# Kernel optimization log

Measured on AMD Instinct MI355X. Metric: run time of the kernel, lower is better.

## Reference

```python
import jax, jax.numpy as jnp
import numpy as np

RES = 64

TRI_TABLE = jnp.array([
    [-1,-1,-1,-1,-1,-1],[1,0,2,-1,-1,-1],[4,0,3,-1,-1,-1],[1,4,2,1,3,4],
    [3,1,5,-1,-1,-1],[2,3,0,2,5,3],[1,4,0,1,5,4],[4,2,5,-1,-1,-1],
    [4,5,2,-1,-1,-1],[4,1,0,4,5,1],[3,2,0,3,5,2],[1,3,5,-1,-1,-1],
    [4,1,2,4,3,1],[3,0,4,-1,-1,-1],[2,0,1,-1,-1,-1],[-1,-1,-1,-1,-1,-1]], dtype=jnp.int32)
NUM_TRI = jnp.array([0,1,1,2,1,2,2,1,1,2,2,1,2,1,1,0], dtype=jnp.int32)
BASE_EDGES = jnp.array([0,1,0,2,0,3,1,2,1,3,2,3], dtype=jnp.int32)


def _make_tet_grid(res):
    # Kuhn 6-tet decomposition of each cube of a (res+1)^3 grid.
    n = res + 1
    ii, jj, kk = np.meshgrid(np.arange(n), np.arange(n), np.arange(n), indexing='ij')
    verts = (np.stack([ii, jj, kk], -1).reshape(-1, 3).astype(np.float32)) / res
    def vid(i, j, k):
        return (i * n + j) * n + k
    i, j, k = np.meshgrid(np.arange(res), np.arange(res), np.arange(res), indexing='ij')
    i, j, k = i.ravel(), j.ravel(), k.ravel()
    c = [vid(i + (b & 1), j + ((b >> 1) & 1), k + ((b >> 2) & 1)) for b in range(8)]
    kuhn = [(0,1,3,7),(0,3,2,7),(0,2,6,7),(0,6,4,7),(0,4,5,7),(0,5,1,7)]
    tets = np.stack([np.stack([c[a], c[b], c[d], c[e]], -1) for (a, b, d, e) in kuhn], 1)
    return verts, tets.reshape(-1, 4).astype(np.int64)


def setup_inputs() -> dict:
    key = jax.random.key(0)
    verts, tets = _make_tet_grid(RES)
    level = jax.random.normal(key, (verts.shape[0], 1), dtype=jnp.float32)
    return {"level": level, "pos": jnp.asarray(verts), "tet": jnp.asarray(tets), "threshold": 0}


def reference(level, pos, tet, threshold):
    sdf = level - threshold                    # [N,1]
    occ = sdf[:, 0] > 0                        # [N]
    occ_fx4 = occ[tet]                         # [F,4]
    occ_sum = occ_fx4.sum(-1)
    valid = (occ_sum > 0) & (occ_sum < 4)
    vt = tet[valid]                            # [Fv,4]
    occ_valid = occ_fx4[valid]                 # [Fv,4]

    edges = jnp.sort(vt[:, BASE_EDGES].reshape(-1, 2), axis=1)   # [Fv*6,2]
    unique_edges, idx_map = jnp.unique(edges, axis=0, return_inverse=True)
    idx_map = idx_map.reshape(-1)
    mask_edges = occ[unique_edges].sum(-1) == 1                  # crossing edges
    mapping = jnp.where(mask_edges, jnp.cumsum(mask_edges) - 1, -1)
    idx_map = mapping[idx_map].reshape(-1, 6)                    # [Fv,6]
    interp_v = unique_edges[mask_edges]                          # [M,2]

    p = pos[interp_v]                                            # [M,2,3]
    s = sdf[interp_v][..., 0] * jnp.array([1.0, -1.0], dtype=sdf.dtype)  # [M,2]
    w = s[:, ::-1] / s.sum(1, keepdims=True)                     # flip / denom
    verts_out = (p * w[..., None]).sum(1)                        # [M,3]

    v_id = 2 ** jnp.arange(4, dtype=jnp.int32)
    tetindex = (occ_valid.astype(jnp.int32) * v_id).sum(-1)      # [Fv]
    num_tri = NUM_TRI[tetindex]
    m1, m2 = num_tri == 1, num_tri == 2
    f1 = jnp.take_along_axis(idx_map[m1], TRI_TABLE[tetindex[m1]][:, :3], axis=1).reshape(-1, 3)
    f2 = jnp.take_along_axis(idx_map[m2], TRI_TABLE[tetindex[m2]][:, :6], axis=1).reshape(-1, 3)
    faces = jnp.concatenate([f1, f2], axis=0)
    return verts_out, faces
```

## Files before the change

### kernel.cpp

```cpp
#include <hip/hip_runtime.h>


#define RESX 64
#define NV   65
#define NV2  4225
#define NVERT 274625
#define NCUBE 262144
#define BLOCK 256
#define NBLK 1073
#define CBLK 1024

__constant__ int c_tri[16][6] = {
    {-1,-1,-1,-1,-1,-1},{1,0,2,-1,-1,-1},{4,0,3,-1,-1,-1},{1,4,2,1,3,4},
    {3,1,5,-1,-1,-1},{2,3,0,2,5,3},{1,4,0,1,5,4},{4,2,5,-1,-1,-1},
    {4,5,2,-1,-1,-1},{4,1,0,4,5,1},{3,2,0,3,5,2},{1,3,5,-1,-1,-1},
    {4,1,2,4,3,1},{3,0,4,-1,-1,-1},{2,0,1,-1,-1,-1},{-1,-1,-1,-1,-1,-1}};
__constant__ int c_ntri[16] = {0,1,1,2,1,2,2,1,1,2,2,1,2,1,1,0};
__constant__ int c_kuhn[6][4] = {{0,1,3,7},{0,3,2,7},{0,2,6,7},{0,6,4,7},{0,4,5,7},{0,5,1,7}};
__constant__ int c_off8[8] = {0,4225,65,4290,1,4226,66,4291};
__constant__ int c_loc[6][6] = {
    {0,0,0,1,1,3},{0,0,0,2,3,2},{0,0,0,2,2,6},
    {0,0,0,4,6,4},{0,0,0,4,4,5},{0,0,0,1,5,1}};
__constant__ int c_dir[6][6] = {
    {3,5,6,1,2,0},{5,1,6,3,0,4},{1,2,6,0,4,3},
    {2,0,6,1,3,5},{0,4,6,3,5,1},{4,3,6,0,1,2}};

__device__ __forceinline__ unsigned block_reduce(unsigned v, unsigned* lds) {
    int tid = threadIdx.x, lane = tid & 63, w = tid >> 6;
#pragma unroll
    for (int off = 32; off > 0; off >>= 1)
        v += (unsigned)__shfl_xor((int)v, off, 64);
    if (lane == 0) lds[w] = v;
    __syncthreads();
    if (tid == 0) lds[4] = lds[0] + lds[1] + lds[2] + lds[3];
    __syncthreads();
    return lds[4];
}

__device__ __forceinline__ unsigned block_scan_excl(unsigned val, unsigned* lds,
                                                    unsigned& block_total) {
    int tid = threadIdx.x, lane = tid & 63, w = tid >> 6;
    unsigned x = val;
#pragma unroll
    for (int off = 1; off < 64; off <<= 1) {
        unsigned y = (unsigned)__shfl_up((int)x, off, 64);
        if (lane >= off) x += y;
    }
    if (lane == 63) lds[w] = x;
    __syncthreads();
    if (tid == 0) {
        unsigned s = 0;
#pragma unroll
        for (int i = 0; i < 4; i++) { unsigned t = lds[i]; lds[i + 4] = s; s += t; }
        lds[8] = s;
    }
    __syncthreads();
    block_total = lds[8];
    return x - val + lds[4 + w];
}

__global__ void pass1(const float* __restrict__ level, const float* __restrict__ thrp,
                      unsigned char* __restrict__ flagsArr,
                      unsigned* __restrict__ bsE,
                      unsigned* __restrict__ bs1, unsigned* __restrict__ bs2) {
    __shared__ unsigned ldsA[5], ldsB[5];
    int tid = threadIdx.x;
    int gid = blockIdx.x * BLOCK + tid;
    float thr = thrp[0];
    unsigned cnt = 0;
    if (gid < NVERT) {
        int i = gid / NV2; int r = gid - i * NV2; int j = r / NV; int k = r - j * NV;
        bool okx = i < RESX, oky = j < RESX, okz = k < RESX;
        float v0 = level[gid] - thr;
        bool s0 = v0 > 0.f;
        unsigned fl = s0 ? 0x80u : 0u;
        const int b2d[8] = {0, 3, 1, 5, 0, 4, 2, 6};
#pragma unroll
        for (int b = 1; b < 8; b++) {
            bool ok = (!(b & 1) || okx) && (!(b & 2) || oky) && (!(b & 4) || okz);
            if (ok) {
                float vb = level[gid + c_off8[b]] - thr;
                if ((vb > 0.f) != s0) fl |= (1u << b2d[b]);
            }
        }
        flagsArr[gid] = (unsigned char)fl;
        cnt = __popc(fl & 0x7fu);
    }
    unsigned totE = block_reduce(cnt, ldsA);
    unsigned tv = 0;
    if (gid < NCUBE) {
        int ci = gid >> 12, cj = (gid >> 6) & 63, ck = gid & 63;
        int base = (ci * NV + cj) * NV + ck;
        unsigned occ8 = 0;
#pragma unroll
        for (int b = 0; b < 8; b++)
            occ8 |= ((level[base + c_off8[b]] - thr) > 0.f ? 1u : 0u) << b;
        unsigned c1 = 0, c2 = 0;
#pragma unroll
        for (int t = 0; t < 6; t++) {
            int cfg = ((occ8 >> c_kuhn[t][0]) & 1) | (((occ8 >> c_kuhn[t][1]) & 1) << 1)
                    | (((occ8 >> c_kuhn[t][2]) & 1) << 2) | (((occ8 >> c_kuhn[t][3]) & 1) << 3);
            int nt = c_ntri[cfg];
            c1 += (nt == 1); c2 += (nt == 2);
        }
        tv = c1 | (c2 << 16);
    }
    unsigned totT = block_reduce(tv, ldsB);
    if (tid == 0) {
        bsE[blockIdx.x] = totE;
        bs1[blockIdx.x] = totT & 0xffffu;
        bs2[blockIdx.x] = totT >> 16;
    }
}

__global__ void scan_partials(unsigned* bsE, unsigned* bs1, unsigned* bs2,
                              unsigned* totals) {
    __shared__ unsigned lds[9];
    unsigned* arr = (blockIdx.x == 0) ? bsE : (blockIdx.x == 1 ? bs1 : bs2);
    unsigned running = 0;
    for (int base = 0; base < NBLK; base += BLOCK) {
        int idx = base + threadIdx.x;
        unsigned v = (idx < NBLK) ? arr[idx] : 0u;
        unsigned tot;
        unsigned ex = block_scan_excl(v, lds, tot);
        if (idx < NBLK) arr[idx] = running + ex;
        running += tot;
        __syncthreads();
    }
    if (threadIdx.x == 0) totals[blockIdx.x] = running;
}

__global__ void emit_verts(const float* __restrict__ level,
                           const float* __restrict__ thrp,
                           const unsigned* __restrict__ bsE,
                           unsigned* __restrict__ base_rank,
                           float* __restrict__ out) {
    __shared__ unsigned lds[9];
    int tid = threadIdx.x;
    int gid = blockIdx.x * BLOCK + tid;
    float thr = thrp[0];
    float v0 = 0.f;
    bool s0 = false;
    float vals[8];
    unsigned fl = 0;
    int i = 0, j = 0, k = 0;
    if (gid < NVERT) {
        i = gid / NV2; int r = gid - i * NV2; j = r / NV; k = r - j * NV;
        bool okx = i < RESX, oky = j < RESX, okz = k < RESX;
        v0 = level[gid] - thr; s0 = v0 > 0.f;
        vals[0] = v0;
        const int b2d[8] = {0, 3, 1, 5, 0, 4, 2, 6};
#pragma unroll
        for (int b = 1; b < 8; b++) {
            bool ok = (!(b & 1) || okx) && (!(b & 2) || oky) && (!(b & 4) || okz);
            float vb = ok ? (level[gid + c_off8[b]] - thr) : 0.f;
            vals[b] = vb;
            if (ok && ((vb > 0.f) != s0)) fl |= (1u << b2d[b]);
        }
    }
    unsigned cnt = __popc(fl & 0x7fu);
    unsigned tot;
    unsigned ex = block_scan_excl(cnt, lds, tot);
    unsigned rank = bsE[blockIdx.x] + ex;
    if (gid < NVERT) base_rank[gid] = rank;
    if (fl & 0x7fu) {
        const float inv = 1.f / 64.f;
        const int d2b[7] = {4, 2, 6, 1, 5, 3, 7};
        float fi = (float)i, fj = (float)j, fk = (float)k;
#pragma unroll
        for (int d = 0; d < 7; d++) {
            if (fl & (1u << d)) {
                const int b = d2b[d];
                float s1 = vals[b];
                float denom = v0 - s1;
                float w0 = (-s1) / denom;
                float w1 = v0 / denom;
                float* o = out + 3u * rank;
                o[0] = (fi * w0 + (fi + (float)(b & 1)) * w1) * inv;
                o[1] = (fj * w0 + (fj + (float)((b >> 1) & 1)) * w1) * inv;
                o[2] = (fk * w0 + (fk + (float)((b >> 2) & 1)) * w1) * inv;
                rank++;
            }
        }
    }
}

__global__ void emit_faces(const unsigned char* __restrict__ flagsArr,
                           const unsigned* __restrict__ base_rank,
                           const unsigned* __restrict__ bs1,
                           const unsigned* __restrict__ bs2,
                           const unsigned* __restrict__ totals,
                           float* __restrict__ out) {
    __shared__ unsigned lds[9];
    int tid = threadIdx.x;
    int gid = blockIdx.x * BLOCK + tid;
    int ci = gid >> 12, cj = (gid >> 6) & 63, ck = gid & 63;
    int base = (ci * NV + cj) * NV + ck;
    unsigned long long f8 = 0ull;
#pragma unroll
    for (int b = 0; b < 8; b++)
        f8 |= (unsigned long long)flagsArr[base + c_off8[b]] << (8 * b);
    unsigned occ8 = 0;
#pragma unroll
    for (int b = 0; b < 8; b++) occ8 |= (unsigned)((f8 >> (8 * b + 7)) & 1ull) << b;
    int cfgs[6], nts[6];
    unsigned c1 = 0, c2 = 0;
#pragma unroll
    for (int t = 0; t < 6; t++) {
        int cfg = ((occ8 >> c_kuhn[t][0]) & 1) | (((occ8 >> c_kuhn[t][1]) & 1) << 1)
                | (((occ8 >> c_kuhn[t][2]) & 1) << 2) | (((occ8 >> c_kuhn[t][3]) & 1) << 3);
        cfgs[t] = cfg;
        int nt = c_ntri[cfg];
        nts[t] = nt;
        c1 += (nt == 1); c2 += (nt == 2);
    }
    unsigned tot;
    unsigned ex = block_scan_excl(c1 | (c2 << 16), lds, tot);
    unsigned p1 = bs1[blockIdx.x] + (ex & 0xffffu);
    unsigned p2 = bs2[blockIdx.x] + (ex >> 16);
    unsigned M = totals[0], C1 = totals[1];
    float* of = out + 3ull * M;
#pragma unroll
    for (int t = 0; t < 6; t++) {
        int nt = nts[t];
        if (nt == 0) continue;
        int cfg = cfgs[t];
        unsigned tri0 = (nt == 1) ? p1 : (C1 + 2u * p2);
        int cntm = 3 * nt;
        for (int m = 0; m < cntm; m++) {
            int e = c_tri[cfg][m];
            int lc = c_loc[t][e];
            int dir = c_dir[t][e];
            int lo = base + c_off8[lc];
            unsigned flb = (unsigned)((f8 >> (8 * lc)) & 0xffull);
            unsigned rank = base_rank[lo] + __popc(flb & ((1u << dir) - 1u));
            of[3u * tri0 + (unsigned)m] = (float)rank;
        }
        p1 += (nt == 1);
        p2 += (nt == 2);
    }
}

extern "C" void kernel_launch(void* const* d_in, const int* in_sizes, int n_in,
                              void* d_out, int out_size, void* d_ws, size_t ws_size,
                              hipStream_t stream) {
    const float* level = (const float*)d_in[0];
    const float* thrp = (const float*)d_in[3];
    float* out = (float*)d_out;

    unsigned char* flagsArr = (unsigned char*)d_ws;
    unsigned* u = (unsigned*)((char*)d_ws + ((NVERT + 255) & ~255));
    unsigned* base_rank = u;
    unsigned* bsE = base_rank + NVERT;
    unsigned* bs1 = bsE + NBLK;
    unsigned* bs2 = bs1 + NBLK;
    unsigned* totals = bs2 + NBLK;

    pass1<<<NBLK, BLOCK, 0, stream>>>(level, thrp, flagsArr, bsE, bs1, bs2);
    scan_partials<<<3, BLOCK, 0, stream>>>(bsE, bs1, bs2, totals);
    emit_verts<<<NBLK, BLOCK, 0, stream>>>(level, thrp, bsE, base_rank, out);
    emit_faces<<<CBLK, BLOCK, 0, stream>>>(flagsArr, base_rank, bs1, bs2, totals, out);
}
```

Baseline: 131.1 us.

## Fuse count, scan and vertex emission into one decoupled-lookback kernel

Merges the counting pass, the separate partial-sum scan kernel and the vertex emission kernel into a single kernel. Blocks publish their edge and triangle counts through status-tagged 64-bit descriptors and compute exclusive prefixes with a wave-wide decoupled lookback. This removes two kernel launches and the second read of the level grid. In exchange it needs a memset of the descriptors and relies on blocks being scheduled in forward order so that spin-waiting cannot deadlock.

```diff
diff --git a/kernel.cpp b/kernel.cpp
--- a/kernel.cpp
+++ b/kernel.cpp
@@ -9,6 +9,8 @@
 #define BLOCK 256
 #define NBLK 1073
 #define CBLK 1024
+
+typedef unsigned long long u64;
 
 __constant__ int c_tri[16][6] = {
     {-1,-1,-1,-1,-1,-1},{1,0,2,-1,-1,-1},{4,0,3,-1,-1,-1},{1,4,2,1,3,4},
@@ -25,6 +27,20 @@
     {3,5,6,1,2,0},{5,1,6,3,0,4},{1,2,6,0,4,3},
     {2,0,6,1,3,5},{0,4,6,3,5,1},{4,3,6,0,1,2}};
 
+__device__ __forceinline__ u64 ld_acq(u64* p) {
+    return __hip_atomic_load(p, __ATOMIC_ACQUIRE, __HIP_MEMORY_SCOPE_AGENT);
+}
+__device__ __forceinline__ void st_rel(u64* p, u64 v) {
+    __hip_atomic_store(p, v, __ATOMIC_RELEASE, __HIP_MEMORY_SCOPE_AGENT);
+}
+
+__device__ __forceinline__ unsigned wave_reduce_add(unsigned v) {
+#pragma unroll
+    for (int off = 32; off; off >>= 1)
+        v += (unsigned)__shfl_xor((int)v, off, 64);
+    return v;
+}
+
 __device__ __forceinline__ unsigned block_reduce(unsigned v, unsigned* lds) {
     int tid = threadIdx.x, lane = tid & 63, w = tid >> 6;
 #pragma unroll
@@ -59,34 +75,79 @@
     return x - val + lds[4 + w];
 }
 
-__global__ void pass1(const float* __restrict__ level, const float* __restrict__ thrp,
-                      unsigned char* __restrict__ flagsArr,
-                      unsigned* __restrict__ bsE,
-                      unsigned* __restrict__ bs1, unsigned* __restrict__ bs2) {
-    __shared__ unsigned ldsA[5], ldsB[5];
+__device__ u64 lookback(u64* desc, int bid, u64 own) {
+    int lane = threadIdx.x & 63;
+    if (bid == 0) {
+        if (lane == 0) st_rel(&desc[0], (2ull << 62) | own);
+        return 0;
+    }
+    if (lane == 0) st_rel(&desc[bid], (1ull << 62) | own);
+    u64 excl = 0;
+    int b = bid;
+    for (;;) {
+        int idx = b - 1 - lane;
+        u64 d;
+        if (idx < 0) d = (2ull << 62);
+        else do { d = ld_acq(&desc[idx]); } while ((d >> 62) == 0);
+        unsigned lo = (unsigned)(d & 0x1fffffu);
+        unsigned hi = (unsigned)((d >> 21) & 0x1fffffu);
+        u64 pmask = __ballot((d >> 62) == 2ull);
+        if (pmask) {
+            int p = __ffsll(pmask) - 1;
+            unsigned ulo = (lane <= p) ? lo : 0u;
+            unsigned uhi = (lane <= p) ? hi : 0u;
+            ulo = wave_reduce_add(ulo);
+            uhi = wave_reduce_add(uhi);
+            excl += (u64)ulo | ((u64)uhi << 21);
+            break;
+        }
+        unsigned ulo = wave_reduce_add(lo);
+        unsigned uhi = wave_reduce_add(hi);
+        excl += (u64)ulo | ((u64)uhi << 21);
+        b -= 64;
+    }
+    if (lane == 0) st_rel(&desc[bid], (2ull << 62) | (excl + own));
+    return excl;
+}
+
+__global__ void __launch_bounds__(256)
+kernelA(const float* __restrict__ level, const float* __restrict__ thrp,
+        unsigned char* __restrict__ flagsArr, unsigned* __restrict__ base_rank,
+        unsigned* __restrict__ bs1, unsigned* __restrict__ bs2,
+        unsigned* __restrict__ totals, u64* descE, u64* descC,
+        float* __restrict__ out) {
+    __shared__ unsigned lds[9];
+    __shared__ unsigned ldsc[5];
+    __shared__ unsigned eexcl_sh;
     int tid = threadIdx.x;
     int gid = blockIdx.x * BLOCK + tid;
     float thr = thrp[0];
-    unsigned cnt = 0;
+
+    float vals[8];
+    unsigned fl = 0;
+    float v0 = 0.f;
+    int i = 0, j = 0, k = 0;
     if (gid < NVERT) {
-        int i = gid / NV2; int r = gid - i * NV2; int j = r / NV; int k = r - j * NV;
+        i = gid / NV2; int r = gid - i * NV2; j = r / NV; k = r - j * NV;
         bool okx = i < RESX, oky = j < RESX, okz = k < RESX;
-        float v0 = level[gid] - thr;
+        v0 = level[gid] - thr;
         bool s0 = v0 > 0.f;
-        unsigned fl = s0 ? 0x80u : 0u;
+        vals[0] = v0;
+        fl = s0 ? 0x80u : 0u;
         const int b2d[8] = {0, 3, 1, 5, 0, 4, 2, 6};
 #pragma unroll
         for (int b = 1; b < 8; b++) {
             bool ok = (!(b & 1) || okx) && (!(b & 2) || oky) && (!(b & 4) || okz);
-            if (ok) {
-                float vb = level[gid + c_off8[b]] - thr;
-                if ((vb > 0.f) != s0) fl |= (1u << b2d[b]);
-            }
+            float vb = ok ? (level[gid + c_off8[b]] - thr) : 0.f;
+            vals[b] = vb;
+            if (ok && ((vb > 0.f) != s0)) fl |= (1u << b2d[b]);
         }
         flagsArr[gid] = (unsigned char)fl;
-        cnt = __popc(fl & 0x7fu);
-    }
-    unsigned totE = block_reduce(cnt, ldsA);
+    }
+    unsigned cnt = __popc(fl & 0x7fu);
+    unsigned totE;
+    unsigned ex = block_scan_excl(cnt, lds, totE);
+
     unsigned tv = 0;
     if (gid < NCUBE) {
         int ci = gid >> 12, cj = (gid >> 6) & 63, ck = gid & 63;
@@ -105,63 +166,28 @@
         }
         tv = c1 | (c2 << 16);
     }
-    unsigned totT = block_reduce(tv, ldsB);
-    if (tid == 0) {
-        bsE[blockIdx.x] = totE;
-        bs1[blockIdx.x] = totT & 0xffffu;
-        bs2[blockIdx.x] = totT >> 16;
-    }
-}
-
-__global__ void scan_partials(unsigned* bsE, unsigned* bs1, unsigned* bs2,
-                              unsigned* totals) {
-    __shared__ unsigned lds[9];
-    unsigned* arr = (blockIdx.x == 0) ? bsE : (blockIdx.x == 1 ? bs1 : bs2);
-    unsigned running = 0;
-    for (int base = 0; base < NBLK; base += BLOCK) {
-        int idx = base + threadIdx.x;
-        unsigned v = (idx < NBLK) ? arr[idx] : 0u;
-        unsigned tot;
-        unsigned ex = block_scan_excl(v, lds, tot);
-        if (idx < NBLK) arr[idx] = running + ex;
-        running += tot;
-        __syncthreads();
-    }
-    if (threadIdx.x == 0) totals[blockIdx.x] = running;
-}
-
-__global__ void emit_verts(const float* __restrict__ level,
-                           const float* __restrict__ thrp,
-                           const unsigned* __restrict__ bsE,
-                           unsigned* __restrict__ base_rank,
-                           float* __restrict__ out) {
-    __shared__ unsigned lds[9];
-    int tid = threadIdx.x;
-    int gid = blockIdx.x * BLOCK + tid;
-    float thr = thrp[0];
-    float v0 = 0.f;
-    bool s0 = false;
-    float vals[8];
-    unsigned fl = 0;
-    int i = 0, j = 0, k = 0;
-    if (gid < NVERT) {
-        i = gid / NV2; int r = gid - i * NV2; j = r / NV; k = r - j * NV;
-        bool okx = i < RESX, oky = j < RESX, okz = k < RESX;
-        v0 = level[gid] - thr; s0 = v0 > 0.f;
-        vals[0] = v0;
-        const int b2d[8] = {0, 3, 1, 5, 0, 4, 2, 6};
-#pragma unroll
-        for (int b = 1; b < 8; b++) {
-            bool ok = (!(b & 1) || okx) && (!(b & 2) || oky) && (!(b & 4) || okz);
-            float vb = ok ? (level[gid + c_off8[b]] - thr) : 0.f;
-            vals[b] = vb;
-            if (ok && ((vb > 0.f) != s0)) fl |= (1u << b2d[b]);
-        }
-    }
-    unsigned cnt = __popc(fl & 0x7fu);
-    unsigned tot;
-    unsigned ex = block_scan_excl(cnt, lds, tot);
-    unsigned rank = bsE[blockIdx.x] + ex;
+    unsigned totC = block_reduce(tv, ldsc);
+
+    int w = tid >> 6;
+    if (w == 0) {
+        u64 e = lookback(descE, blockIdx.x, (u64)totE);
+        if ((tid & 63) == 0) {
+            eexcl_sh = (unsigned)e;
+            if (blockIdx.x == NBLK - 1) totals[0] = (unsigned)e + totE;
+        }
+    } else if (w == 1 && blockIdx.x < CBLK) {
+        u64 pay = (u64)(totC & 0xffffu) | ((u64)(totC >> 16) << 21);
+        u64 c = lookback(descC, blockIdx.x, pay);
+        if ((tid & 63) == 0) {
+            bs1[blockIdx.x] = (unsigned)(c & 0x1fffffu);
+            bs2[blockIdx.x] = (unsigned)((c >> 21) & 0x1fffffu);
+            if (blockIdx.x == CBLK - 1)
+                totals[1] = (unsigned)((c + pay) & 0x1fffffu);
+        }
+    }
+    __syncthreads();
+
+    unsigned rank = eexcl_sh + ex;
     if (gid < NVERT) base_rank[gid] = rank;
     if (fl & 0x7fu) {
         const float inv = 1.f / 64.f;
@@ -185,12 +211,11 @@
     }
 }
 
-__global__ void emit_faces(const unsigned char* __restrict__ flagsArr,
-                           const unsigned* __restrict__ base_rank,
-                           const unsigned* __restrict__ bs1,
-                           const unsigned* __restrict__ bs2,
-                           const unsigned* __restrict__ totals,
-                           float* __restrict__ out) {
+__global__ void __launch_bounds__(256)
+emit_faces(const unsigned char* __restrict__ flagsArr,
+           const unsigned* __restrict__ base_rank,
+           const unsigned* __restrict__ bs1, const unsigned* __restrict__ bs2,
+           const unsigned* __restrict__ totals, float* __restrict__ out) {
     __shared__ unsigned lds[9];
     int tid = threadIdx.x;
     int gid = blockIdx.x * BLOCK + tid;
@@ -248,16 +273,22 @@
     const float* thrp = (const float*)d_in[3];
     float* out = (float*)d_out;
 
-    unsigned char* flagsArr = (unsigned char*)d_ws;
-    unsigned* u = (unsigned*)((char*)d_ws + ((NVERT + 255) & ~255));
-    unsigned* base_rank = u;
-    unsigned* bsE = base_rank + NVERT;
-    unsigned* bs1 = bsE + NBLK;
-    unsigned* bs2 = bs1 + NBLK;
-    unsigned* totals = bs2 + NBLK;
-
-    pass1<<<NBLK, BLOCK, 0, stream>>>(level, thrp, flagsArr, bsE, bs1, bs2);
-    scan_partials<<<3, BLOCK, 0, stream>>>(bsE, bs1, bs2, totals);
-    emit_verts<<<NBLK, BLOCK, 0, stream>>>(level, thrp, bsE, base_rank, out);
-    emit_faces<<<CBLK, BLOCK, 0, stream>>>(flagsArr, base_rank, bs1, bs2, totals, out);
-}
+    char* p = (char*)d_ws;
+    unsigned char* flagsArr = (unsigned char*)p;
+    p += (NVERT + 255) & ~255;
+    unsigned* base_rank = (unsigned*)p; p += sizeof(unsigned) * NVERT;
+    unsigned* bs1 = (unsigned*)p;       p += sizeof(unsigned) * CBLK;
+    unsigned* bs2 = (unsigned*)p;       p += sizeof(unsigned) * CBLK;
+    p = (char*)(((uintptr_t)p + 7) & ~(uintptr_t)7);
+    char* zero_base = p;
+    u64* descE = (u64*)p;               p += sizeof(u64) * NBLK;
+    u64* descC = (u64*)p;               p += sizeof(u64) * CBLK;
+    unsigned* totals = (unsigned*)p;    p += sizeof(unsigned) * 8;
+    size_t zbytes = (size_t)(p - zero_base);
+
+    hipMemsetAsync(zero_base, 0, zbytes, stream);
+    kernelA<<<NBLK, BLOCK, 0, stream>>>(level, thrp, flagsArr, base_rank,
+                                        bs1, bs2, totals, descE, descC, out);
+    emit_faces<<<CBLK, BLOCK, 0, stream>>>(flagsArr, base_rank, bs1, bs2,
+                                           totals, out);
+}
```

After: 288.9 us. +120.3%, slower.

## Fuse partial scan and emit kernels into two-pass scheme with per-block redundant reductions

Applied to the files above, without the earlier changes.

Collapses four launches into two. The first pass stores each vertex's in-block exclusive edge offset as a 16-bit value next to the block totals. The second pass has every block redundantly reduce all block partials to get its own prefixes and the global counts, then emits vertices and faces in the same kernel. Face ranks come from a small shared window of block prefixes plus the local offsets, so the 32-bit base_rank array and the separate scan kernel are no longer needed. The cost is redundant partial-sum reads in every block and the assumption that the face neighbourhood spans at most WINW vertex blocks.

```diff
diff --git a/kernel.cpp b/kernel.cpp
--- a/kernel.cpp
+++ b/kernel.cpp
@@ -9,6 +9,7 @@
 #define BLOCK 256
 #define NBLK 1073
 #define CBLK 1024
+#define WINW 20
 
 __constant__ int c_tri[16][6] = {
     {-1,-1,-1,-1,-1,-1},{1,0,2,-1,-1,-1},{4,0,3,-1,-1,-1},{1,4,2,1,3,4},
@@ -59,21 +60,24 @@
     return x - val + lds[4 + w];
 }
 
-__global__ void pass1(const float* __restrict__ level, const float* __restrict__ thrp,
-                      unsigned char* __restrict__ flagsArr,
-                      unsigned* __restrict__ bsE,
-                      unsigned* __restrict__ bs1, unsigned* __restrict__ bs2) {
-    __shared__ unsigned ldsA[5], ldsB[5];
+__global__ void __launch_bounds__(256)
+pass1(const float* __restrict__ level, const float* __restrict__ thrp,
+      unsigned char* __restrict__ flagsArr, unsigned short* __restrict__ locEx,
+      unsigned* __restrict__ bsE, unsigned* __restrict__ bsT) {
+    __shared__ unsigned lds[9];
+    __shared__ unsigned ldsc[5];
     int tid = threadIdx.x;
-    int gid = blockIdx.x * BLOCK + tid;
+    int bid = blockIdx.x;
+    int gid = bid * BLOCK + tid;
     float thr = thrp[0];
-    unsigned cnt = 0;
+
+    unsigned fl = 0;
     if (gid < NVERT) {
         int i = gid / NV2; int r = gid - i * NV2; int j = r / NV; int k = r - j * NV;
         bool okx = i < RESX, oky = j < RESX, okz = k < RESX;
         float v0 = level[gid] - thr;
         bool s0 = v0 > 0.f;
-        unsigned fl = s0 ? 0x80u : 0u;
+        fl = s0 ? 0x80u : 0u;
         const int b2d[8] = {0, 3, 1, 5, 0, 4, 2, 6};
 #pragma unroll
         for (int b = 1; b < 8; b++) {
@@ -84,9 +88,13 @@
             }
         }
         flagsArr[gid] = (unsigned char)fl;
-        cnt = __popc(fl & 0x7fu);
-    }
-    unsigned totE = block_reduce(cnt, ldsA);
+    }
+    unsigned cnt = __popc(fl & 0x7fu);
+    unsigned totE;
+    unsigned ex = block_scan_excl(cnt, lds, totE);
+    if (gid < NVERT) locEx[gid] = (unsigned short)ex;
+    if (tid == 0) bsE[bid] = totE;
+
     unsigned tv = 0;
     if (gid < NCUBE) {
         int ci = gid >> 12, cj = (gid >> 6) & 63, ck = gid & 63;
@@ -105,95 +113,80 @@
         }
         tv = c1 | (c2 << 16);
     }
-    unsigned totT = block_reduce(tv, ldsB);
-    if (tid == 0) {
-        bsE[blockIdx.x] = totE;
-        bs1[blockIdx.x] = totT & 0xffffu;
-        bs2[blockIdx.x] = totT >> 16;
-    }
-}
-
-__global__ void scan_partials(unsigned* bsE, unsigned* bs1, unsigned* bs2,
-                              unsigned* totals) {
+    unsigned totC = block_reduce(tv, ldsc);
+    if (tid == 0) bsT[bid] = totC;
+}
+
+__global__ void __launch_bounds__(256)
+pass2(const float* __restrict__ level, const float* __restrict__ thrp,
+      const unsigned char* __restrict__ flagsArr,
+      const unsigned short* __restrict__ locEx,
+      const unsigned* __restrict__ bsE, const unsigned* __restrict__ bsT,
+      float* __restrict__ out) {
     __shared__ unsigned lds[9];
-    unsigned* arr = (blockIdx.x == 0) ? bsE : (blockIdx.x == 1 ? bs1 : bs2);
-    unsigned running = 0;
-    for (int base = 0; base < NBLK; base += BLOCK) {
-        int idx = base + threadIdx.x;
-        unsigned v = (idx < NBLK) ? arr[idx] : 0u;
-        unsigned tot;
-        unsigned ex = block_scan_excl(v, lds, tot);
-        if (idx < NBLK) arr[idx] = running + ex;
-        running += tot;
-        __syncthreads();
-    }
-    if (threadIdx.x == 0) totals[blockIdx.x] = running;
-}
-
-__global__ void emit_verts(const float* __restrict__ level,
-                           const float* __restrict__ thrp,
-                           const unsigned* __restrict__ bsE,
-                           unsigned* __restrict__ base_rank,
-                           float* __restrict__ out) {
-    __shared__ unsigned lds[9];
+    __shared__ unsigned ldsc[5];
+    __shared__ unsigned pEw[WINW];
     int tid = threadIdx.x;
-    int gid = blockIdx.x * BLOCK + tid;
+    int bid = blockIdx.x;
+    int gid = bid * BLOCK + tid;
     float thr = thrp[0];
-    float v0 = 0.f;
-    bool s0 = false;
-    float vals[8];
-    unsigned fl = 0;
-    int i = 0, j = 0, k = 0;
+
+    int g0 = bid << 8;
+    int wci = g0 >> 12, wcj = (g0 >> 6) & 63;
+    int base0 = (wci * NV + wcj) * NV;
+    int wb = (bid < CBLK) ? (base0 >> 8) : 0;
+
+    unsigned lE = 0, lEp = 0, lWb = 0, l1 = 0, l1p = 0, l2p = 0;
+    for (int t = tid; t < NBLK; t += BLOCK) {
+        unsigned e = bsE[t], c = bsT[t];
+        lE += e; l1 += c & 0xffffu;
+        if (t < bid) { lEp += e; l1p += c & 0xffffu; l2p += c >> 16; }
+        if (t < wb)  { lWb += e; }
+    }
+    unsigned M    = block_reduce(lE,  ldsc);
+    unsigned pE   = block_reduce(lEp, ldsc);
+    unsigned C1   = block_reduce(l1,  ldsc);
+    unsigned p1b  = block_reduce(l1p, ldsc);
+    unsigned p2b  = block_reduce(l2p, ldsc);
+    unsigned wAcc = block_reduce(lWb, ldsc);
+    if (tid < WINW) {
+        unsigned s = wAcc;
+        for (int d = 0; d < tid; d++) {
+            int t = wb + d;
+            s += (t < NBLK) ? bsE[t] : 0u;
+        }
+        pEw[tid] = s;
+    }
+    __syncthreads();
+
     if (gid < NVERT) {
-        i = gid / NV2; int r = gid - i * NV2; j = r / NV; k = r - j * NV;
-        bool okx = i < RESX, oky = j < RESX, okz = k < RESX;
-        v0 = level[gid] - thr; s0 = v0 > 0.f;
-        vals[0] = v0;
-        const int b2d[8] = {0, 3, 1, 5, 0, 4, 2, 6};
-#pragma unroll
-        for (int b = 1; b < 8; b++) {
-            bool ok = (!(b & 1) || okx) && (!(b & 2) || oky) && (!(b & 4) || okz);
-            float vb = ok ? (level[gid + c_off8[b]] - thr) : 0.f;
-            vals[b] = vb;
-            if (ok && ((vb > 0.f) != s0)) fl |= (1u << b2d[b]);
-        }
-    }
-    unsigned cnt = __popc(fl & 0x7fu);
-    unsigned tot;
-    unsigned ex = block_scan_excl(cnt, lds, tot);
-    unsigned rank = bsE[blockIdx.x] + ex;
-    if (gid < NVERT) base_rank[gid] = rank;
-    if (fl & 0x7fu) {
-        const float inv = 1.f / 64.f;
-        const int d2b[7] = {4, 2, 6, 1, 5, 3, 7};
-        float fi = (float)i, fj = (float)j, fk = (float)k;
-#pragma unroll
-        for (int d = 0; d < 7; d++) {
-            if (fl & (1u << d)) {
-                const int b = d2b[d];
-                float s1 = vals[b];
-                float denom = v0 - s1;
-                float w0 = (-s1) / denom;
-                float w1 = v0 / denom;
-                float* o = out + 3u * rank;
-                o[0] = (fi * w0 + (fi + (float)(b & 1)) * w1) * inv;
-                o[1] = (fj * w0 + (fj + (float)((b >> 1) & 1)) * w1) * inv;
-                o[2] = (fk * w0 + (fk + (float)((b >> 2) & 1)) * w1) * inv;
-                rank++;
+        unsigned fl = flagsArr[gid];
+        if (fl & 0x7fu) {
+            int i = gid / NV2; int r = gid - i * NV2; int j = r / NV; int k = r - j * NV;
+            float v0 = level[gid] - thr;
+            unsigned rank = pE + locEx[gid];
+            const float inv = 1.f / 64.f;
+            const int d2b[7] = {4, 2, 6, 1, 5, 3, 7};
+            float fi = (float)i, fj = (float)j, fk = (float)k;
+#pragma unroll
+            for (int d = 0; d < 7; d++) {
+                if (fl & (1u << d)) {
+                    const int b = d2b[d];
+                    float s1 = level[gid + c_off8[b]] - thr;
+                    float denom = v0 - s1;
+                    float w0 = (-s1) / denom;
+                    float w1 = v0 / denom;
+                    float* o = out + 3u * rank;
+                    o[0] = (fi * w0 + (fi + (float)(b & 1)) * w1) * inv;
+                    o[1] = (fj * w0 + (fj + (float)((b >> 1) & 1)) * w1) * inv;
+                    o[2] = (fk * w0 + (fk + (float)((b >> 2) & 1)) * w1) * inv;
+                    rank++;
+                }
             }
         }
     }
-}
-
-__global__ void emit_faces(const unsigned char* __restrict__ flagsArr,
-                           const unsigned* __restrict__ base_rank,
-                           const unsigned* __restrict__ bs1,
-                           const unsigned* __restrict__ bs2,
-                           const unsigned* __restrict__ totals,
-                           float* __restrict__ out) {
-    __shared__ unsigned lds[9];
-    int tid = threadIdx.x;
-    int gid = blockIdx.x * BLOCK + tid;
+
+    if (bid >= CBLK) return;
     int ci = gid >> 12, cj = (gid >> 6) & 63, ck = gid & 63;
     int base = (ci * NV + cj) * NV + ck;
     unsigned long long f8 = 0ull;
@@ -214,11 +207,10 @@
         nts[t] = nt;
         c1 += (nt == 1); c2 += (nt == 2);
     }
-    unsigned tot;
-    unsigned ex = block_scan_excl(c1 | (c2 << 16), lds, tot);
-    unsigned p1 = bs1[blockIdx.x] + (ex & 0xffffu);
-    unsigned p2 = bs2[blockIdx.x] + (ex >> 16);
-    unsigned M = totals[0], C1 = totals[1];
+    unsigned tot2;
+    unsigned ex2 = block_scan_excl(c1 | (c2 << 16), lds, tot2);
+    unsigned p1 = p1b + (ex2 & 0xffffu);
+    unsigned p2 = p2b + (ex2 >> 16);
     float* of = out + 3ull * M;
 #pragma unroll
     for (int t = 0; t < 6; t++) {
@@ -233,8 +225,9 @@
             int dir = c_dir[t][e];
             int lo = base + c_off8[lc];
             unsigned flb = (unsigned)((f8 >> (8 * lc)) & 0xffull);
-            unsigned rank = base_rank[lo] + __popc(flb & ((1u << dir) - 1u));
-            of[3u * tri0 + (unsigned)m] = (float)rank;
+            unsigned rnk = pEw[(lo >> 8) - wb] + locEx[lo]
+                         + __popc(flb & ((1u << dir) - 1u));
+            of[3u * tri0 + (unsigned)m] = (float)rnk;
         }
         p1 += (nt == 1);
         p2 += (nt == 2);
@@ -248,16 +241,14 @@
     const float* thrp = (const float*)d_in[3];
     float* out = (float*)d_out;
 
-    unsigned char* flagsArr = (unsigned char*)d_ws;
-    unsigned* u = (unsigned*)((char*)d_ws + ((NVERT + 255) & ~255));
-    unsigned* base_rank = u;
-    unsigned* bsE = base_rank + NVERT;
-    unsigned* bs1 = bsE + NBLK;
-    unsigned* bs2 = bs1 + NBLK;
-    unsigned* totals = bs2 + NBLK;
-
-    pass1<<<NBLK, BLOCK, 0, stream>>>(level, thrp, flagsArr, bsE, bs1, bs2);
-    scan_partials<<<3, BLOCK, 0, stream>>>(bsE, bs1, bs2, totals);
-    emit_verts<<<NBLK, BLOCK, 0, stream>>>(level, thrp, bsE, base_rank, out);
-    emit_faces<<<CBLK, BLOCK, 0, stream>>>(flagsArr, base_rank, bs1, bs2, totals, out);
-}
+    char* p = (char*)d_ws;
+    unsigned char* flagsArr = (unsigned char*)p;
+    p += (NVERT + 255) & ~255;
+    unsigned short* locEx = (unsigned short*)p;
+    p += ((sizeof(unsigned short) * NVERT) + 255) & ~255;
+    unsigned* bsE = (unsigned*)p;  p += sizeof(unsigned) * NBLK;
+    unsigned* bsT = (unsigned*)p;
+
+    pass1<<<NBLK, BLOCK, 0, stream>>>(level, thrp, flagsArr, locEx, bsE, bsT);
+    pass2<<<NBLK, BLOCK, 0, stream>>>(level, thrp, flagsArr, locEx, bsE, bsT, out);
+}
```

Result: faster. 123.4 us (-5.9%).
